# Optimization experiments

Hardware: AMD Instinct MI355X
Metric: run time of the kernel (lower is better)

## Reference

```python
import jax, jax.numpy as jnp
import numpy as np

C1, C2, C3, C4, C5 = 20, 100, 500, 2000, 10000
FEAT, B = 512, 8192
# parent maps (stand-ins for l1_to_l2..l4_to_l5 group lists): child c -> parent c // fanout
P5 = jnp.arange(C5) // 5   # l5 class -> l4 group
P4 = jnp.arange(C4) // 4   # l4 class -> l3 group
P3 = jnp.arange(C3) // 5   # l3 class -> l2 group
P2 = jnp.arange(C2) // 5   # l2 class -> l1 group


def _l2norm(w):
    # F.normalize(w, p=2, dim=1)
    return w / jnp.maximum(jnp.linalg.norm(w, axis=1, keepdims=True), 1e-12)


def _jsd(p, q, eps=1e-8):
    # Jensen-Shannon divergence between row-wise distributions, mean over batch
    m = 0.5 * (p + q)
    log_m = jnp.log(m + eps)
    kl_pm = jnp.sum(p * (jnp.log(p + eps) - log_m), axis=1)
    kl_qm = jnp.sum(q * (jnp.log(q + eps) - log_m), axis=1)
    return jnp.mean(0.5 * (kl_pm + kl_qm))


def setup_inputs() -> dict:
    key = jax.random.key(0)
    k = jax.random.split(key, 8)
    s = 0.02
    return {
        "x": jax.random.normal(k[0], (B, FEAT), jnp.float32),
        "targets": jax.random.randint(k[1], (B,), 0, C5, jnp.int32),
        "W1": jax.random.normal(k[2], (C1, FEAT), jnp.float32) * s,
        "b1": jnp.zeros((C1,), jnp.float32),
        "W2": jax.random.normal(k[3], (C2, FEAT), jnp.float32) * s,
        "b2": jnp.zeros((C2,), jnp.float32),
        "W3": jax.random.normal(k[4], (C3, FEAT), jnp.float32) * s,
        "b3": jnp.zeros((C3,), jnp.float32),
        "W4": jax.random.normal(k[5], (C4, FEAT), jnp.float32) * s,
        "b4": jnp.zeros((C4,), jnp.float32),
        "W5": jax.random.normal(k[6], (C5, FEAT), jnp.float32) * s,
        "b5": jnp.zeros((C5,), jnp.float32),
    }


def reference(x, targets, W1, b1, W2, b2, W3, b3, W4, b4, W5, b5):
    # row-normalized classifier weights (second F.normalize in the original is idempotent)
    w1, w2, w3, w4, w5 = (_l2norm(W1), _l2norm(W2), _l2norm(W3), _l2norm(W4), _l2norm(W5))
    l1 = x @ w1.T + b1
    l2 = x @ w2.T + b2
    l3 = x @ w3.T + b3
    l4 = x @ w4.T + b4
    l5 = x @ w5.T + b5  # [B, C5]

    # cross-entropy on finest level logits
    logp5 = jax.nn.log_softmax(l5, axis=1)
    ce_loss = -jnp.mean(jnp.take_along_axis(logp5, targets[:, None].astype(jnp.int32), axis=1)[:, 0])

    p1 = jax.nn.softmax(l1, axis=1)
    p2 = jax.nn.softmax(l2, axis=1)
    p3 = jax.nn.softmax(l3, axis=1)
    p4 = jax.nn.softmax(l4, axis=1)
    p5 = jax.nn.softmax(l5, axis=1)

    # hierarchy-aggregated weights: segment-sum child rows, renormalize, cosine vs parent
    def agg_cos(parent_w, child_w, seg, num_seg):
        hat = _l2norm(jax.ops.segment_sum(child_w, seg, num_segments=num_seg))
        return jnp.mean(jnp.sum(parent_w * hat, axis=1))  # rows are unit norm -> cosine

    l2_w_45 = agg_cos(w4, w5, P5, C4)
    l2_w_34 = agg_cos(w3, w4, P4, C3)
    l2_w_23 = agg_cos(w2, w3, P3, C2)
    l2_w_12 = agg_cos(w1, w2, P2, C1)

    # hierarchy-aggregated probabilities: column segment-sums, then JSD vs parent
    def agg_prob(child_p, seg, num_seg):
        return jax.ops.segment_sum(child_p.T, seg, num_segments=num_seg).T

    jsd_45 = _jsd(agg_prob(p5, P5, C4), p4)
    jsd_34 = _jsd(agg_prob(p4, P4, C3), p3)
    jsd_23 = _jsd(agg_prob(p3, P3, C2), p2)
    jsd_12 = _jsd(agg_prob(p2, P2, C1), p1)

    loss = ce_loss + (jsd_45 + jsd_34 + jsd_23 + jsd_12) - (l2_w_45 + l2_w_34 + l2_w_23 + l2_w_12)
    return p5, loss
```

## Files before the change

kernel.cpp:

```cpp
#include <hip/hip_runtime.h>
#include <hip/hip_bf16.h>
#include <stdint.h>

typedef unsigned short u16;
typedef __bf16 bf16x8 __attribute__((ext_vector_type(8)));
typedef float f32x4 __attribute__((ext_vector_type(4)));

#define FEAT 512
#define BATCH 8192
#define NC1 20
#define NC2 100
#define NC3 500
#define NC4 2000
#define NC5 10000
#define NCAT 2620
#define LDP 2624
#define NTOT 12620

__device__ inline u16 f2bf(float f) {
    unsigned int u = __builtin_bit_cast(unsigned int, f);
    unsigned int r = (u + 0x7FFFu + ((u >> 16) & 1u)) >> 16;
    return (u16)r;
}
__device__ inline float bfu(u16 u) {
    return __builtin_bit_cast(float, (unsigned int)u << 16);
}

__device__ inline float waveReduceSum(float v) {
    #pragma unroll
    for (int off = 32; off > 0; off >>= 1) v += __shfl_xor(v, off);
    return v;
}
__device__ inline float waveReduceMax(float v) {
    #pragma unroll
    for (int off = 32; off > 0; off >>= 1) v = fmaxf(v, __shfl_xor(v, off));
    return v;
}
__device__ inline float blockReduceSum(float v, float* sh) {
    int t = threadIdx.x;
    v = waveReduceSum(v);
    __syncthreads();
    if ((t & 63) == 0) sh[t >> 6] = v;
    __syncthreads();
    return sh[0] + sh[1] + sh[2] + sh[3];
}
__device__ inline float blockReduceMax(float v, float* sh) {
    int t = threadIdx.x;
    v = waveReduceMax(v);
    __syncthreads();
    if ((t & 63) == 0) sh[t >> 6] = v;
    __syncthreads();
    return fmaxf(fmaxf(sh[0], sh[1]), fmaxf(sh[2], sh[3]));
}

__device__ inline void gload16(const void* g, void* l) {
    __builtin_amdgcn_global_load_lds((const __attribute__((address_space(1))) void*)g,
                                     (__attribute__((address_space(3))) void*)l, 16, 0, 0);
}


__global__ __launch_bounds__(256) void cast_x(const float* __restrict__ x, u16* __restrict__ xb, int n8) {
    int i = blockIdx.x * blockDim.x + threadIdx.x;
    if (i >= n8) return;
    const float* p = x + (size_t)i * 8;
    union { u16 u[8]; uint4 v; } o;
    #pragma unroll
    for (int j = 0; j < 8; ++j) o.u[j] = f2bf(p[j]);
    ((uint4*)xb)[i] = o.v;
}

__global__ __launch_bounds__(64) void wnorm_all(const float* __restrict__ W1, const float* __restrict__ b1,
                                                const float* __restrict__ W2, const float* __restrict__ b2,
                                                const float* __restrict__ W3, const float* __restrict__ b3,
                                                const float* __restrict__ W4, const float* __restrict__ b4,
                                                const float* __restrict__ W5, const float* __restrict__ b5,
                                                u16* __restrict__ wb, float* __restrict__ biascat) {
    int r = blockIdx.x;
    const float* W; const float* b; int lr;
    if      (r < 20)   { W = W1; b = b1; lr = r; }
    else if (r < 120)  { W = W2; b = b2; lr = r - 20; }
    else if (r < 620)  { W = W3; b = b3; lr = r - 120; }
    else if (r < 2620) { W = W4; b = b4; lr = r - 620; }
    else               { W = W5; b = b5; lr = r - 2620; }
    int t = threadIdx.x;
    const float* p = W + (size_t)lr * FEAT + t * 8;
    float v[8]; float ss = 0.f;
    #pragma unroll
    for (int j = 0; j < 8; ++j) { v[j] = p[j]; ss += v[j] * v[j]; }
    ss = waveReduceSum(ss);
    float inv = 1.0f / fmaxf(sqrtf(ss), 1e-12f);
    union { u16 u[8]; uint4 q; } o;
    #pragma unroll
    for (int j = 0; j < 8; ++j) o.u[j] = f2bf(v[j] * inv);
    ((uint4*)(wb + (size_t)r * FEAT))[t] = o.q;
    if (t == 0) biascat[r] = b[lr];
}


#define BM 256
#define BN 256
#define BK 64
#define KITERS (FEAT / BK)

template <bool STATS>
__global__ __launch_bounds__(512, 2) void gemm_bt(const u16* __restrict__ A, const u16* __restrict__ Bw,
                                                  const float* __restrict__ bias, u16* __restrict__ C,
                                                  int N, int ldc,
                                                  float* __restrict__ pmax, float* __restrict__ psum, int nct) {
    __shared__ u16 sAB[2][2 * BM * BK];
    const int t = threadIdx.x;
    const int lane = t & 63, wid = t >> 6;
    const int lane15 = lane & 15, q = lane >> 4;
    const int wr = wid >> 2, wcol = wid & 3;

    int nwg = gridDim.x * gridDim.y;
    int lid = blockIdx.y * gridDim.x + blockIdx.x;
    int cpx = nwg >> 3;
    int swz = (lid & 7) * cpx + (lid >> 3);
    int bx = swz % gridDim.x, by = swz / gridDim.x;
    const int r0 = bx * BM, c0 = by * BN;

    f32x4 acc[8][4];
    #pragma unroll
    for (int m = 0; m < 8; ++m)
        #pragma unroll
        for (int n = 0; n < 4; ++n) acc[m][n] = f32x4{0.f, 0.f, 0.f, 0.f};

    auto stage = [&](int kt, int buf) {
        char* base = (char*)sAB[buf];
        #pragma unroll
        for (int p = 0; p < 8; ++p) {
            int chunk = p * 512 + t;
            int row = chunk >> 3, blk = chunk & 7;
            int srck = 8 * (blk ^ (row & 7));
            const u16* g;
            if (p < 4) {
                g = A + (size_t)(r0 + row) * FEAT + kt + srck;
            } else {
                int brow = c0 + (row - 256); if (brow >= N) brow = N - 1;
                g = Bw + (size_t)brow * FEAT + kt + srck;
            }
            gload16(g, base + (size_t)chunk * 16);
        }
    };

    stage(0, 0);
    stage(BK, 1);
    for (int ki = 0; ki < KITERS; ++ki) {
        if (ki + 1 < KITERS) { asm volatile("s_waitcnt vmcnt(8)" ::: "memory"); }
        else                 { asm volatile("s_waitcnt vmcnt(0)" ::: "memory"); }
        __builtin_amdgcn_sched_barrier(0);
        __builtin_amdgcn_s_barrier();
        __builtin_amdgcn_sched_barrier(0);
        char* sAb = (char*)sAB[ki & 1];
        char* sBb = sAb + BM * BK * 2;
        #pragma unroll
        for (int ks = 0; ks < 2; ++ks) {
            const int kko = ks * 4 + q;
            bf16x8 af[8], bv[4];
            #pragma unroll
            for (int m = 0; m < 8; ++m) {
                int row = wr * 128 + m * 16 + lane15;
                af[m] = *reinterpret_cast<const bf16x8*>(sAb + row * 128 + 16 * (kko ^ (row & 7)));
            }
            #pragma unroll
            for (int n = 0; n < 4; ++n) {
                int row = wcol * 64 + n * 16 + lane15;
                bv[n] = *reinterpret_cast<const bf16x8*>(sBb + row * 128 + 16 * (kko ^ (row & 7)));
            }
            #pragma unroll
            for (int m = 0; m < 8; ++m)
                #pragma unroll
                for (int n = 0; n < 4; ++n)
                    acc[m][n] = __builtin_amdgcn_mfma_f32_16x16x32_bf16(bv[n], af[m], acc[m][n], 0, 0, 0);
        }
        __builtin_amdgcn_sched_barrier(0);
        __builtin_amdgcn_s_barrier();
        __builtin_amdgcn_sched_barrier(0);
        if (ki + 2 < KITERS) stage((ki + 2) * BK, ki & 1);
    }

    bool vld[4]; int cb[4];
    #pragma unroll
    for (int n = 0; n < 4; ++n) {
        cb[n] = c0 + wcol * 64 + n * 16 + q * 4;
        vld[n] = (cb[n] < N);
        if (vld[n]) {
            float b0 = bias[cb[n]], b1 = bias[cb[n] + 1], b2 = bias[cb[n] + 2], b3 = bias[cb[n] + 3];
            #pragma unroll
            for (int m = 0; m < 8; ++m) {
                acc[m][n][0] += b0; acc[m][n][1] += b1;
                acc[m][n][2] += b2; acc[m][n][3] += b3;
            }
        }
    }

    if (STATS) {
        float* fmx = (float*)sAB;
        float* fsm = fmx + 1024;
        float bm[8];
        #pragma unroll
        for (int m = 0; m < 8; ++m) {
            float v = -1e30f;
            #pragma unroll
            for (int n = 0; n < 4; ++n)
                if (vld[n]) {
                    #pragma unroll
                    for (int j = 0; j < 4; ++j) v = fmaxf(v, acc[m][n][j]);
                }
            v = fmaxf(v, __shfl_xor(v, 16));
            v = fmaxf(v, __shfl_xor(v, 32));
            bm[m] = v;
        }
        if (lane < 16) {
            #pragma unroll
            for (int m = 0; m < 8; ++m)
                fmx[(wr * 128 + m * 16 + lane15) * 4 + wcol] = bm[m];
        }
        __syncthreads();
        #pragma unroll
        for (int m = 0; m < 8; ++m) {
            int row = wr * 128 + m * 16 + lane15;
            bm[m] = fmaxf(fmaxf(fmx[row * 4], fmx[row * 4 + 1]),
                          fmaxf(fmx[row * 4 + 2], fmx[row * 4 + 3]));
        }
        float sm[8];
        #pragma unroll
        for (int m = 0; m < 8; ++m) {
            float s = 0.f;
            #pragma unroll
            for (int n = 0; n < 4; ++n)
                if (vld[n]) {
                    #pragma unroll
                    for (int j = 0; j < 4; ++j) s += __expf(acc[m][n][j] - bm[m]);
                }
            s += __shfl_xor(s, 16);
            s += __shfl_xor(s, 32);
            sm[m] = s;
        }
        if (lane < 16) {
            #pragma unroll
            for (int m = 0; m < 8; ++m)
                fsm[(wr * 128 + m * 16 + lane15) * 4 + wcol] = sm[m];
        }
        __syncthreads();
        if (t < 256) {
            float m4 = fmaxf(fmaxf(fmx[t * 4], fmx[t * 4 + 1]), fmaxf(fmx[t * 4 + 2], fmx[t * 4 + 3]));
            float s4 = fsm[t * 4] + fsm[t * 4 + 1] + fsm[t * 4 + 2] + fsm[t * 4 + 3];
            size_t idx = (size_t)(r0 + t) * nct + by;
            pmax[idx] = m4;
            psum[idx] = s4;
        }
    }

    #pragma unroll
    for (int m = 0; m < 8; ++m) {
        int row = r0 + wr * 128 + m * 16 + lane15;
        #pragma unroll
        for (int n = 0; n < 4; ++n) {
            if (vld[n]) {
                union { u16 u[4]; uint2 v; } pk;
                #pragma unroll
                for (int j = 0; j < 4; ++j) pk.u[j] = f2bf(acc[m][n][j]);
                *reinterpret_cast<uint2*>(&C[(size_t)row * ldc + cb[n]]) = pk.v;
            }
        }
    }
}


__global__ __launch_bounds__(256) void probs_all(const u16* __restrict__ l5b, float* __restrict__ out,
                                                 const u16* __restrict__ pcat,
                                                 const float* __restrict__ pmax, const float* __restrict__ psum,
                                                 int nct, const int* __restrict__ tgt,
                                                 float* __restrict__ cerow,
                                                 float* __restrict__ j12, float* __restrict__ j23,
                                                 float* __restrict__ j34, float* __restrict__ j45) {
    __shared__ u16 P5[NC5];
    __shared__ float PC[LDP];
    __shared__ float sh[4];
    __shared__ float shls;
    int b = blockIdx.x, t = threadIdx.x;
    float* orow = out + (size_t)b * NC5;
    const u16* lrow = l5b + (size_t)b * NC5;
    const u16* prow = pcat + (size_t)b * LDP;

    if (t < 64) {
        float pm = (t < nct) ? pmax[(size_t)b * nct + t] : -1e30f;
        float ps = (t < nct) ? psum[(size_t)b * nct + t] : 0.f;
        float gm = waveReduceMax(pm);
        float s = waveReduceSum(ps * __expf(pm - gm));
        if (t == 0) {
            float ls = gm + __logf(s);
            shls = ls;
            int tg = tgt[b];
            cerow[b] = -(bfu(lrow[tg]) - ls);
        }
    }
    for (int c = t; c < LDP / 8; c += 256) {
        uint4 raw = ((const uint4*)prow)[c];
        const u16* rp = (const u16*)&raw;
        #pragma unroll
        for (int k = 0; k < 8; ++k) PC[c * 8 + k] = bfu(rp[k]);
    }
    __syncthreads();
    float ls = shls;

    for (int c = t; c < NC5 / 8; c += 256) {
        uint4 raw = ((const uint4*)lrow)[c];
        const u16* rp = (const u16*)&raw;
        f32x4 p0, p1;
        #pragma unroll
        for (int k = 0; k < 4; ++k) p0[k] = __expf(bfu(rp[k]) - ls);
        #pragma unroll
        for (int k = 0; k < 4; ++k) p1[k] = __expf(bfu(rp[4 + k]) - ls);
        ((f32x4*)orow)[c * 2] = p0;
        ((f32x4*)orow)[c * 2 + 1] = p1;
        union { u16 u[8]; uint4 v; } pk;
        #pragma unroll
        for (int k = 0; k < 4; ++k) pk.u[k] = f2bf(p0[k]);
        #pragma unroll
        for (int k = 0; k < 4; ++k) pk.u[4 + k] = f2bf(p1[k]);
        ((uint4*)P5)[c] = pk.v;
    }
    __syncthreads();

    auto softmax_seg = [&](int off, int C) {
        float m = -1e30f;
        for (int c = t; c < C; c += 256) m = fmaxf(m, PC[off + c]);
        m = blockReduceMax(m, sh);
        float s = 0.f;
        for (int c = t; c < C; c += 256) { float e = __expf(PC[off + c] - m); PC[off + c] = e; s += e; }
        s = blockReduceSum(s, sh);
        float inv = 1.0f / s;
        for (int c = t; c < C; c += 256) PC[off + c] *= inv;
    };
    softmax_seg(0, NC1);
    softmax_seg(20, NC2);
    softmax_seg(120, NC3);
    softmax_seg(620, NC4);
    __syncthreads();

    {
        float klpm = 0.f, klqm = 0.f;
        for (int g = t; g < NC4; g += 256) {
            float qv = 0.f;
            #pragma unroll
            for (int f = 0; f < 5; ++f) qv += bfu(P5[5 * g + f]);
            float pp = PC[620 + g];
            float mm = 0.5f * (qv + pp);
            float lm = __logf(mm + 1e-8f);
            klpm += qv * (__logf(qv + 1e-8f) - lm);
            klqm += pp * (__logf(pp + 1e-8f) - lm);
        }
        float tot = blockReduceSum(0.5f * (klpm + klqm), sh);
        if (t == 0) j45[b] = tot;
    }
    auto jsd_seg = [&](int childOff, int fan, int parentOff, int nPar, float* dst) {
        float klpm = 0.f, klqm = 0.f;
        for (int g = t; g < nPar; g += 256) {
            float qv = 0.f;
            for (int f = 0; f < fan; ++f) qv += PC[childOff + g * fan + f];
            float pp = PC[parentOff + g];
            float mm = 0.5f * (qv + pp);
            float lm = __logf(mm + 1e-8f);
            klpm += qv * (__logf(qv + 1e-8f) - lm);
            klqm += pp * (__logf(pp + 1e-8f) - lm);
        }
        float tot = blockReduceSum(0.5f * (klpm + klqm), sh);
        if (t == 0) dst[b] = tot;
    };
    jsd_seg(620, 4, 120, NC3, j34);
    jsd_seg(120, 5, 20, NC2, j23);
    jsd_seg(20, 5, 0, NC1, j12);
}


__global__ __launch_bounds__(64) void wcos_all(const float* __restrict__ W1, const float* __restrict__ W2,
                                               const float* __restrict__ W3, const float* __restrict__ W4,
                                               const float* __restrict__ W5,
                                               float* __restrict__ c45, float* __restrict__ c34,
                                               float* __restrict__ c23, float* __restrict__ c12) {
    int g = blockIdx.x; int t = threadIdx.x;
    const float* Wp; const float* Wc; int fan; float* dst; int j;
    if      (g < 2000) { Wp = W4; Wc = W5; fan = 5; dst = c45; j = g; }
    else if (g < 2500) { Wp = W3; Wc = W4; fan = 4; dst = c34; j = g - 2000; }
    else if (g < 2600) { Wp = W2; Wc = W3; fan = 5; dst = c23; j = g - 2500; }
    else               { Wp = W1; Wc = W2; fan = 5; dst = c12; j = g - 2600; }

    float hat[8] = {0, 0, 0, 0, 0, 0, 0, 0};
    for (int c = 0; c < fan; ++c) {
        const float* cr = Wc + ((size_t)(j * fan + c)) * FEAT + t * 8;
        float v[8]; float ss = 0.f;
        #pragma unroll
        for (int i = 0; i < 8; ++i) { v[i] = cr[i]; ss += v[i] * v[i]; }
        ss = waveReduceSum(ss);
        float inv = 1.0f / fmaxf(sqrtf(ss), 1e-12f);
        #pragma unroll
        for (int i = 0; i < 8; ++i) hat[i] += v[i] * inv;
    }
    float hs = 0.f;
    #pragma unroll
    for (int i = 0; i < 8; ++i) hs += hat[i] * hat[i];
    hs = waveReduceSum(hs);
    float hinv = 1.0f / fmaxf(sqrtf(hs), 1e-12f);
    const float* pr = Wp + (size_t)j * FEAT + t * 8;
    float ps = 0.f, dot = 0.f;
    #pragma unroll
    for (int i = 0; i < 8; ++i) { float pv = pr[i]; ps += pv * pv; dot += pv * hat[i]; }
    ps = waveReduceSum(ps);
    dot = waveReduceSum(dot);
    if (t == 0) dst[j] = dot * hinv / fmaxf(sqrtf(ps), 1e-12f);
}

__global__ __launch_bounds__(256) void finalize(const float* __restrict__ ce, const float* __restrict__ j45,
                                                const float* __restrict__ j34, const float* __restrict__ j23,
                                                const float* __restrict__ j12, const float* __restrict__ c45,
                                                const float* __restrict__ c34, const float* __restrict__ c23,
                                                const float* __restrict__ c12, float* __restrict__ lossOut) {
    __shared__ float sh[4];
    auto meanArr = [&](const float* a, int n) {
        float s = 0.f;
        for (int i = threadIdx.x; i < n; i += 256) s += a[i];
        s = blockReduceSum(s, sh);
        return s / n;
    };
    float loss = meanArr(ce, BATCH);
    loss += meanArr(j45, BATCH) + meanArr(j34, BATCH) + meanArr(j23, BATCH) + meanArr(j12, BATCH);
    loss -= meanArr(c45, NC4) + meanArr(c34, NC3) + meanArr(c23, NC2) + meanArr(c12, NC1);
    if (threadIdx.x == 0) *lossOut = loss;
}


extern "C" void kernel_launch(void* const* d_in, const int* in_sizes, int n_in,
                              void* d_out, int out_size, void* d_ws, size_t ws_size,
                              hipStream_t stream) {
    const float* x  = (const float*)d_in[0];
    const int*   tg = (const int*)d_in[1];
    const float* W1 = (const float*)d_in[2];  const float* b1 = (const float*)d_in[3];
    const float* W2 = (const float*)d_in[4];  const float* b2 = (const float*)d_in[5];
    const float* W3 = (const float*)d_in[6];  const float* b3 = (const float*)d_in[7];
    const float* W4 = (const float*)d_in[8];  const float* b4 = (const float*)d_in[9];
    const float* W5 = (const float*)d_in[10]; const float* b5 = (const float*)d_in[11];
    float* out = (float*)d_out;

    const int NCT = (NC5 + BN - 1) / BN;

    char* ws = (char*)d_ws;
    size_t off = 0;
    auto alloc = [&](size_t bytes) { void* p = ws + off; off = (off + bytes + 255) & ~(size_t)255; return p; };
    u16*   xb      = (u16*)alloc((size_t)BATCH * FEAT * 2);
    u16*   wb      = (u16*)alloc((size_t)NTOT * FEAT * 2);
    float* biascat = (float*)alloc((size_t)NTOT * 4);
    u16*   pcat    = (u16*)alloc((size_t)BATCH * LDP * 2);
    u16*   l5b     = (u16*)alloc((size_t)BATCH * NC5 * 2);
    float* pmax    = (float*)alloc((size_t)BATCH * NCT * 4);
    float* psum    = (float*)alloc((size_t)BATCH * NCT * 4);
    float* cerow   = (float*)alloc((size_t)BATCH * 4);
    float* j45     = (float*)alloc((size_t)BATCH * 4);
    float* j34     = (float*)alloc((size_t)BATCH * 4);
    float* j23     = (float*)alloc((size_t)BATCH * 4);
    float* j12     = (float*)alloc((size_t)BATCH * 4);
    float* c45     = (float*)alloc((size_t)NC4 * 4);
    float* c34     = (float*)alloc((size_t)NC3 * 4);
    float* c23     = (float*)alloc((size_t)NC2 * 4);
    float* c12     = (float*)alloc((size_t)NC1 * 4);

    cast_x<<<(BATCH * FEAT / 8 + 255) / 256, 256, 0, stream>>>(x, xb, BATCH * FEAT / 8);
    wnorm_all<<<NTOT, 64, 0, stream>>>(W1, b1, W2, b2, W3, b3, W4, b4, W5, b5, wb, biascat);

    gemm_bt<false><<<dim3(BATCH / BM, (NCAT + BN - 1) / BN), 512, 0, stream>>>(
        xb, wb, biascat, pcat, NCAT, LDP, nullptr, nullptr, 0);
    gemm_bt<true><<<dim3(BATCH / BM, NCT), 512, 0, stream>>>(
        xb, wb + (size_t)NCAT * FEAT, biascat + NCAT, l5b, NC5, NC5, pmax, psum, NCT);

    probs_all<<<BATCH, 256, 0, stream>>>(l5b, out, pcat, pmax, psum, NCT, tg, cerow,
                                         j12, j23, j34, j45);

    wcos_all<<<NC4 + NC3 + NC2 + NC1, 64, 0, stream>>>(W1, W2, W3, W4, W5, c45, c34, c23, c12);

    finalize<<<1, 256, 0, stream>>>(cerow, j45, j34, j23, j12, c45, c34, c23, c12,
                                    out + (size_t)BATCH * NC5);
}
```

Baseline: 414.9 us.

## Fuse prep kernels and both GEMMs, reuse bf16 weights for cosine terms

Merges the x cast and weight normalization into one prep launch. Merges the coarse-level and level-5 GEMMs into a single grid over all 12620 columns. Each output tile is routed to pcat or l5b, and softmax stats are masked to level-5 columns. It also brackets the MFMA loop with s_setprio, uses nontemporal loads and stores in probs_all, and makes wcos_all read the already-normalized bf16 weights instead of renormalizing the fp32 rows. The aim is fewer launches, a smaller GEMM tail and less weight traffic; the cost is reduced precision in the cosine terms.

```diff
diff --git a/kernel.cpp b/kernel.cpp
--- a/kernel.cpp
+++ b/kernel.cpp
@@ -5,6 +5,7 @@
 typedef unsigned short u16;
 typedef __bf16 bf16x8 __attribute__((ext_vector_type(8)));
 typedef float f32x4 __attribute__((ext_vector_type(4)));
+typedef unsigned int u32x4 __attribute__((ext_vector_type(4)));
 
 #define FEAT 512
 #define BATCH 8192
@@ -16,6 +17,8 @@
 #define NCAT 2620
 #define LDP 2624
 #define NTOT 12620
+#define WN_BLOCKS 3155
+#define CAST_BLOCKS 2048
 
 __device__ inline u16 f2bf(float f) {
     unsigned int u = __builtin_bit_cast(unsigned int, f);
@@ -59,41 +62,43 @@
 }
 
 
-__global__ __launch_bounds__(256) void cast_x(const float* __restrict__ x, u16* __restrict__ xb, int n8) {
-    int i = blockIdx.x * blockDim.x + threadIdx.x;
-    if (i >= n8) return;
-    const float* p = x + (size_t)i * 8;
-    union { u16 u[8]; uint4 v; } o;
-    #pragma unroll
-    for (int j = 0; j < 8; ++j) o.u[j] = f2bf(p[j]);
-    ((uint4*)xb)[i] = o.v;
-}
-
-__global__ __launch_bounds__(64) void wnorm_all(const float* __restrict__ W1, const float* __restrict__ b1,
-                                                const float* __restrict__ W2, const float* __restrict__ b2,
-                                                const float* __restrict__ W3, const float* __restrict__ b3,
-                                                const float* __restrict__ W4, const float* __restrict__ b4,
-                                                const float* __restrict__ W5, const float* __restrict__ b5,
-                                                u16* __restrict__ wb, float* __restrict__ biascat) {
-    int r = blockIdx.x;
-    const float* W; const float* b; int lr;
-    if      (r < 20)   { W = W1; b = b1; lr = r; }
-    else if (r < 120)  { W = W2; b = b2; lr = r - 20; }
-    else if (r < 620)  { W = W3; b = b3; lr = r - 120; }
-    else if (r < 2620) { W = W4; b = b4; lr = r - 620; }
-    else               { W = W5; b = b5; lr = r - 2620; }
-    int t = threadIdx.x;
-    const float* p = W + (size_t)lr * FEAT + t * 8;
-    float v[8]; float ss = 0.f;
-    #pragma unroll
-    for (int j = 0; j < 8; ++j) { v[j] = p[j]; ss += v[j] * v[j]; }
-    ss = waveReduceSum(ss);
-    float inv = 1.0f / fmaxf(sqrtf(ss), 1e-12f);
-    union { u16 u[8]; uint4 q; } o;
-    #pragma unroll
-    for (int j = 0; j < 8; ++j) o.u[j] = f2bf(v[j] * inv);
-    ((uint4*)(wb + (size_t)r * FEAT))[t] = o.q;
-    if (t == 0) biascat[r] = b[lr];
+__global__ __launch_bounds__(256) void prep(const float* __restrict__ x, u16* __restrict__ xb,
+                                            const float* __restrict__ W1, const float* __restrict__ b1,
+                                            const float* __restrict__ W2, const float* __restrict__ b2,
+                                            const float* __restrict__ W3, const float* __restrict__ b3,
+                                            const float* __restrict__ W4, const float* __restrict__ b4,
+                                            const float* __restrict__ W5, const float* __restrict__ b5,
+                                            u16* __restrict__ wb, float* __restrict__ biascat) {
+    int bid = blockIdx.x;
+    if (bid < WN_BLOCKS) {
+        int r = bid * 4 + (threadIdx.x >> 6);
+        if (r >= NTOT) return;
+        int t = threadIdx.x & 63;
+        const float* W; const float* b; int lr;
+        if      (r < 20)   { W = W1; b = b1; lr = r; }
+        else if (r < 120)  { W = W2; b = b2; lr = r - 20; }
+        else if (r < 620)  { W = W3; b = b3; lr = r - 120; }
+        else if (r < 2620) { W = W4; b = b4; lr = r - 620; }
+        else               { W = W5; b = b5; lr = r - 2620; }
+        const float* p = W + (size_t)lr * FEAT + t * 8;
+        float v[8]; float ss = 0.f;
+        #pragma unroll
+        for (int j = 0; j < 8; ++j) { v[j] = p[j]; ss += v[j] * v[j]; }
+        ss = waveReduceSum(ss);
+        float inv = 1.0f / fmaxf(sqrtf(ss), 1e-12f);
+        union { u16 u[8]; uint4 q; } o;
+        #pragma unroll
+        for (int j = 0; j < 8; ++j) o.u[j] = f2bf(v[j] * inv);
+        ((uint4*)(wb + (size_t)r * FEAT))[t] = o.q;
+        if (t == 0) biascat[r] = b[lr];
+    } else {
+        int i = (bid - WN_BLOCKS) * 256 + threadIdx.x;
+        const float* p = x + (size_t)i * 8;
+        union { u16 u[8]; uint4 v; } o;
+        #pragma unroll
+        for (int j = 0; j < 8; ++j) o.u[j] = f2bf(p[j]);
+        ((uint4*)xb)[i] = o.v;
+    }
 }
 
 
@@ -102,11 +107,10 @@
 #define BK 64
 #define KITERS (FEAT / BK)
 
-template <bool STATS>
-__global__ __launch_bounds__(512, 2) void gemm_bt(const u16* __restrict__ A, const u16* __restrict__ Bw,
-                                                  const float* __restrict__ bias, u16* __restrict__ C,
-                                                  int N, int ldc,
-                                                  float* __restrict__ pmax, float* __restrict__ psum, int nct) {
+__global__ __launch_bounds__(512, 2) void gemm_all(const u16* __restrict__ A, const u16* __restrict__ Bw,
+                                                   const float* __restrict__ bias,
+                                                   u16* __restrict__ pcat, u16* __restrict__ l5b,
+                                                   float* __restrict__ pmax, float* __restrict__ psum) {
     __shared__ u16 sAB[2][2 * BM * BK];
     const int t = threadIdx.x;
     const int lane = t & 63, wid = t >> 6;
@@ -137,7 +141,7 @@
             if (p < 4) {
                 g = A + (size_t)(r0 + row) * FEAT + kt + srck;
             } else {
-                int brow = c0 + (row - 256); if (brow >= N) brow = N - 1;
+                int brow = c0 + (row - 256); if (brow >= NTOT) brow = NTOT - 1;
                 g = Bw + (size_t)brow * FEAT + kt + srck;
             }
             gload16(g, base + (size_t)chunk * 16);
@@ -168,11 +172,13 @@
                 int row = wcol * 64 + n * 16 + lane15;
                 bv[n] = *reinterpret_cast<const bf16x8*>(sBb + row * 128 + 16 * (kko ^ (row & 7)));
             }
+            __builtin_amdgcn_s_setprio(1);
             #pragma unroll
             for (int m = 0; m < 8; ++m)
                 #pragma unroll
                 for (int n = 0; n < 4; ++n)
                     acc[m][n] = __builtin_amdgcn_mfma_f32_16x16x32_bf16(bv[n], af[m], acc[m][n], 0, 0, 0);
+            __builtin_amdgcn_s_setprio(0);
         }
         __builtin_amdgcn_sched_barrier(0);
         __builtin_amdgcn_s_barrier();
@@ -180,11 +186,12 @@
         if (ki + 2 < KITERS) stage((ki + 2) * BK, ki & 1);
     }
 
-    bool vld[4]; int cb[4];
+    bool vld[4], svld[4]; int cb[4];
     #pragma unroll
     for (int n = 0; n < 4; ++n) {
         cb[n] = c0 + wcol * 64 + n * 16 + q * 4;
-        vld[n] = (cb[n] < N);
+        vld[n] = (cb[n] < NTOT);
+        svld[n] = vld[n] && (cb[n] >= NCAT);
         if (vld[n]) {
             float b0 = bias[cb[n]], b1 = bias[cb[n] + 1], b2 = bias[cb[n] + 2], b3 = bias[cb[n] + 3];
             #pragma unroll
@@ -195,7 +202,7 @@
         }
     }
 
-    if (STATS) {
+    if (by >= 10) {
         float* fmx = (float*)sAB;
         float* fsm = fmx + 1024;
         float bm[8];
@@ -204,7 +211,7 @@
             float v = -1e30f;
             #pragma unroll
             for (int n = 0; n < 4; ++n)
-                if (vld[n]) {
+                if (svld[n]) {
                     #pragma unroll
                     for (int j = 0; j < 4; ++j) v = fmaxf(v, acc[m][n][j]);
                 }
@@ -230,7 +237,7 @@
             float s = 0.f;
             #pragma unroll
             for (int n = 0; n < 4; ++n)
-                if (vld[n]) {
+                if (svld[n]) {
                     #pragma unroll
                     for (int j = 0; j < 4; ++j) s += __expf(acc[m][n][j] - bm[m]);
                 }
@@ -247,7 +254,7 @@
         if (t < 256) {
             float m4 = fmaxf(fmaxf(fmx[t * 4], fmx[t * 4 + 1]), fmaxf(fmx[t * 4 + 2], fmx[t * 4 + 3]));
             float s4 = fsm[t * 4] + fsm[t * 4 + 1] + fsm[t * 4 + 2] + fsm[t * 4 + 3];
-            size_t idx = (size_t)(r0 + t) * nct + by;
+            size_t idx = (size_t)(r0 + t) * 40 + (by - 10);
             pmax[idx] = m4;
             psum[idx] = s4;
         }
@@ -262,7 +269,10 @@
                 union { u16 u[4]; uint2 v; } pk;
                 #pragma unroll
                 for (int j = 0; j < 4; ++j) pk.u[j] = f2bf(acc[m][n][j]);
-                *reinterpret_cast<uint2*>(&C[(size_t)row * ldc + cb[n]]) = pk.v;
+                u16* dst = (cb[n] < NCAT)
+                    ? &pcat[(size_t)row * LDP + cb[n]]
+                    : &l5b[(size_t)row * NC5 + (cb[n] - NCAT)];
+                *reinterpret_cast<uint2*>(dst) = pk.v;
             }
         }
     }
@@ -298,7 +308,7 @@
         }
     }
     for (int c = t; c < LDP / 8; c += 256) {
-        uint4 raw = ((const uint4*)prow)[c];
+        u32x4 raw = __builtin_nontemporal_load(&((const u32x4*)prow)[c]);
         const u16* rp = (const u16*)&raw;
         #pragma unroll
         for (int k = 0; k < 8; ++k) PC[c * 8 + k] = bfu(rp[k]);
@@ -307,15 +317,15 @@
     float ls = shls;
 
     for (int c = t; c < NC5 / 8; c += 256) {
-        uint4 raw = ((const uint4*)lrow)[c];
+        u32x4 raw = __builtin_nontemporal_load(&((const u32x4*)lrow)[c]);
         const u16* rp = (const u16*)&raw;
         f32x4 p0, p1;
         #pragma unroll
         for (int k = 0; k < 4; ++k) p0[k] = __expf(bfu(rp[k]) - ls);
         #pragma unroll
         for (int k = 0; k < 4; ++k) p1[k] = __expf(bfu(rp[4 + k]) - ls);
-        ((f32x4*)orow)[c * 2] = p0;
-        ((f32x4*)orow)[c * 2 + 1] = p1;
+        __builtin_nontemporal_store(p0, &((f32x4*)orow)[c * 2]);
+        __builtin_nontemporal_store(p1, &((f32x4*)orow)[c * 2 + 1]);
         union { u16 u[8]; uint4 v; } pk;
         #pragma unroll
         for (int k = 0; k < 4; ++k) pk.u[k] = f2bf(p0[k]);
@@ -376,41 +386,35 @@
 }
 
 
-__global__ __launch_bounds__(64) void wcos_all(const float* __restrict__ W1, const float* __restrict__ W2,
-                                               const float* __restrict__ W3, const float* __restrict__ W4,
-                                               const float* __restrict__ W5,
+__global__ __launch_bounds__(64) void wcos_all(const u16* __restrict__ wb,
                                                float* __restrict__ c45, float* __restrict__ c34,
                                                float* __restrict__ c23, float* __restrict__ c12) {
     int g = blockIdx.x; int t = threadIdx.x;
-    const float* Wp; const float* Wc; int fan; float* dst; int j;
-    if      (g < 2000) { Wp = W4; Wc = W5; fan = 5; dst = c45; j = g; }
-    else if (g < 2500) { Wp = W3; Wc = W4; fan = 4; dst = c34; j = g - 2000; }
-    else if (g < 2600) { Wp = W2; Wc = W3; fan = 5; dst = c23; j = g - 2500; }
-    else               { Wp = W1; Wc = W2; fan = 5; dst = c12; j = g - 2600; }
+    int pOff, cOff, fan, j; float* dst;
+    if      (g < 2000) { pOff = 620; cOff = 2620; fan = 5; dst = c45; j = g; }
+    else if (g < 2500) { pOff = 120; cOff = 620;  fan = 4; dst = c34; j = g - 2000; }
+    else if (g < 2600) { pOff = 20;  cOff = 120;  fan = 5; dst = c23; j = g - 2500; }
+    else               { pOff = 0;   cOff = 20;   fan = 5; dst = c12; j = g - 2600; }
 
     float hat[8] = {0, 0, 0, 0, 0, 0, 0, 0};
     for (int c = 0; c < fan; ++c) {
-        const float* cr = Wc + ((size_t)(j * fan + c)) * FEAT + t * 8;
-        float v[8]; float ss = 0.f;
-        #pragma unroll
-        for (int i = 0; i < 8; ++i) { v[i] = cr[i]; ss += v[i] * v[i]; }
-        ss = waveReduceSum(ss);
-        float inv = 1.0f / fmaxf(sqrtf(ss), 1e-12f);
-        #pragma unroll
-        for (int i = 0; i < 8; ++i) hat[i] += v[i] * inv;
+        const uint4 raw = ((const uint4*)(wb + (size_t)(cOff + j * fan + c) * FEAT))[t];
+        const u16* rp = (const u16*)&raw;
+        #pragma unroll
+        for (int i = 0; i < 8; ++i) hat[i] += bfu(rp[i]);
     }
     float hs = 0.f;
     #pragma unroll
     for (int i = 0; i < 8; ++i) hs += hat[i] * hat[i];
     hs = waveReduceSum(hs);
     float hinv = 1.0f / fmaxf(sqrtf(hs), 1e-12f);
-    const float* pr = Wp + (size_t)j * FEAT + t * 8;
-    float ps = 0.f, dot = 0.f;
-    #pragma unroll
-    for (int i = 0; i < 8; ++i) { float pv = pr[i]; ps += pv * pv; dot += pv * hat[i]; }
-    ps = waveReduceSum(ps);
+    const uint4 praw = ((const uint4*)(wb + (size_t)(pOff + j) * FEAT))[t];
+    const u16* pp = (const u16*)&praw;
+    float dot = 0.f;
+    #pragma unroll
+    for (int i = 0; i < 8; ++i) dot += bfu(pp[i]) * hat[i];
     dot = waveReduceSum(dot);
-    if (t == 0) dst[j] = dot * hinv / fmaxf(sqrtf(ps), 1e-12f);
+    if (t == 0) dst[j] = dot * hinv;
 }
 
 __global__ __launch_bounds__(256) void finalize(const float* __restrict__ ce, const float* __restrict__ j45,
@@ -444,7 +448,7 @@
     const float* W5 = (const float*)d_in[10]; const float* b5 = (const float*)d_in[11];
     float* out = (float*)d_out;
 
-    const int NCT = (NC5 + BN - 1) / BN;
+    const int NCT = 40;
 
     char* ws = (char*)d_ws;
     size_t off = 0;
@@ -466,18 +470,16 @@
     float* c23     = (float*)alloc((size_t)NC2 * 4);
     float* c12     = (float*)alloc((size_t)NC1 * 4);
 
-    cast_x<<<(BATCH * FEAT / 8 + 255) / 256, 256, 0, stream>>>(x, xb, BATCH * FEAT / 8);
-    wnorm_all<<<NTOT, 64, 0, stream>>>(W1, b1, W2, b2, W3, b3, W4, b4, W5, b5, wb, biascat);
-
-    gemm_bt<false><<<dim3(BATCH / BM, (NCAT + BN - 1) / BN), 512, 0, stream>>>(
-        xb, wb, biascat, pcat, NCAT, LDP, nullptr, nullptr, 0);
-    gemm_bt<true><<<dim3(BATCH / BM, NCT), 512, 0, stream>>>(
-        xb, wb + (size_t)NCAT * FEAT, biascat + NCAT, l5b, NC5, NC5, pmax, psum, NCT);
+    prep<<<WN_BLOCKS + CAST_BLOCKS, 256, 0, stream>>>(x, xb, W1, b1, W2, b2, W3, b3, W4, b4, W5, b5,
+                                                      wb, biascat);
+
+    gemm_all<<<dim3(BATCH / BM, (NTOT + BN - 1) / BN), 512, 0, stream>>>(
+        xb, wb, biascat, pcat, l5b, pmax, psum);
 
     probs_all<<<BATCH, 256, 0, stream>>>(l5b, out, pcat, pmax, psum, NCT, tg, cerow,
                                          j12, j23, j34, j45);
 
-    wcos_all<<<NC4 + NC3 + NC2 + NC1, 64, 0, stream>>>(W1, W2, W3, W4, W5, c45, c34, c23, c12);
+    wcos_all<<<NC4 + NC3 + NC2 + NC1, 64, 0, stream>>>(wb, c45, c34, c23, c12);
 
     finalize<<<1, 256, 0, stream>>>(cerow, j45, j34, j23, j12, c45, c34, c23, c12,
                                     out + (size_t)BATCH * NC5);
```

Result: faster. 391.9 us (-5.6%).
